# Performance work log

Measured on AMD Instinct MI355X. Metric: run time of the kernel, lower is better.

The kernel has to match this reference:

```python
import jax, jax.numpy as jnp
import numpy as np

T = 2048      # num_tokens = batch*seq
H = 2048      # hidden_size
E = 64        # num_experts
K = 8         # num_experts_per_tok (top_k)
I = 768       # moe_intermediate_size


def setup_inputs() -> dict:
    key = jax.random.key(0)
    k0, k1, k2, k3, k4 = jax.random.split(key, 5)
    scale = 0.02
    return {
        "hidden_states": jax.random.normal(k0, (T, H), jnp.float32),
        "w_router": jax.random.normal(k1, (E, H), jnp.float32) * scale,   # gate Linear [E, H]
        "w_gate": jax.random.normal(k2, (E, I, H), jnp.float32) * scale,  # per-expert gate_proj
        "w_up": jax.random.normal(k3, (E, I, H), jnp.float32) * scale,    # per-expert up_proj
        "w_down": jax.random.normal(k4, (E, H, I), jnp.float32) * scale,  # per-expert down_proj
    }


def reference(hidden_states, w_router, w_gate, w_up, w_down):
    x = hidden_states                                  # [T, H]
    num_tokens = x.shape[0]
    # --- router ---
    router_logits = x @ w_router.T                     # [T, E]
    probs = jax.nn.softmax(router_logits.astype(jnp.float32), axis=-1)
    top_w, top_i = jax.lax.top_k(probs, K)             # [T, K]
    top_w = top_w / jnp.sum(top_w, axis=-1, keepdims=True)  # norm_topk_prob
    top_w = top_w.astype(x.dtype)
    # dense combine weights [T, E], K nonzeros per row
    combine = jnp.zeros((num_tokens, E), x.dtype).at[
        jnp.arange(num_tokens)[:, None], top_i
    ].set(top_w)
    # --- experts: SwiGLU MLP per expert, weighted combine ---
    def body(acc, params):
        wg, wu, wd, w_e = params                       # [I,H], [I,H], [H,I], [T]
        h = jax.nn.silu(x @ wg.T) * (x @ wu.T)         # [T, I]
        return acc + w_e[:, None] * (h @ wd.T), None
    out, _ = jax.lax.scan(body, jnp.zeros_like(x), (w_gate, w_up, w_down, combine.T))
    return out
```

## Files before the change

kernel.cpp:

```cpp
#include <hip/hip_runtime.h>
#include <hip/hip_fp16.h>

#define T_TOK 2048
#define H_DIM 2048
#define E_NUM 64
#define TOPK  8
#define I_DIM 768

#define BK   32

#define GU_MT 3
#define GU_NT (I_DIM / 64)
#define GU_NWG (GU_MT * GU_NT * E_NUM)
#define DN_MT 3
#define DN_NT (H_DIM / 128)
#define DN_NWG (DN_MT * DN_NT * E_NUM)

using f16x8 = __attribute__((ext_vector_type(8))) _Float16;
using f16x4 = __attribute__((ext_vector_type(4))) _Float16;
using f16x2 = __attribute__((ext_vector_type(2))) _Float16;
using f32x4 = __attribute__((ext_vector_type(4))) float;

__device__ __forceinline__ f16x4 cvt4(float4 v) {
    f16x2 lo = __builtin_bit_cast(f16x2, __builtin_amdgcn_cvt_pkrtz(v.x, v.y));
    f16x2 hi = __builtin_bit_cast(f16x2, __builtin_amdgcn_cvt_pkrtz(v.z, v.w));
    f16x4 o;
    o[0] = lo[0]; o[1] = lo[1]; o[2] = hi[0]; o[3] = hi[1];
    return o;
}
__device__ __forceinline__ f16x8 cvt8(float4 a, float4 b) {
    f16x4 lo = cvt4(a), hi = cvt4(b);
    f16x8 r;
    r[0] = lo[0]; r[1] = lo[1]; r[2] = lo[2]; r[3] = lo[3];
    r[4] = hi[0]; r[5] = hi[1]; r[6] = hi[2]; r[7] = hi[3];
    return r;
}

__device__ __forceinline__ void gload16(const void* g, void* l) {
    __builtin_amdgcn_global_load_lds(
        (const __attribute__((address_space(1))) unsigned int*)g,
        (__attribute__((address_space(3))) unsigned int*)l,
        16, 0, 0);
}

__global__ void convert_x_kernel(const float* __restrict__ x, _Float16* __restrict__ xh, int n) {
    int i = (blockIdx.x * blockDim.x + threadIdx.x) * 4;
    if (i < n) {
        float4 v = *reinterpret_cast<const float4*>(x + i);
        *reinterpret_cast<f16x4*>(xh + i) = cvt4(v);
    }
}

__global__ __launch_bounds__(64) void router_topk_kernel(
        const float* __restrict__ x, const float* __restrict__ wr,
        int* __restrict__ topk_i, float* __restrict__ topk_w) {
    __shared__ float xs[H_DIM];
    int t = blockIdx.x;
    int lane = threadIdx.x;
    const float* xp = x + (size_t)t * H_DIM;
    for (int i = lane * 4; i < H_DIM; i += 64 * 4) {
        *reinterpret_cast<float4*>(xs + i) = *reinterpret_cast<const float4*>(xp + i);
    }
    __syncthreads();
    const float* wp = wr + (size_t)lane * H_DIM;
    float acc = 0.f;
    for (int h = 0; h < H_DIM; h += 4) {
        float4 w = *reinterpret_cast<const float4*>(wp + h);
        acc += xs[h] * w.x + xs[h + 1] * w.y + xs[h + 2] * w.z + xs[h + 3] * w.w;
    }
    float m = acc;
    #pragma unroll
    for (int d = 32; d; d >>= 1) m = fmaxf(m, __shfl_xor(m, d));
    float p = __expf(acc - m);
    float s = p;
    #pragma unroll
    for (int d = 32; d; d >>= 1) s += __shfl_xor(s, d);
    p /= s;
    float selv[TOPK]; int seli[TOPK];
    float cur = p;
    #pragma unroll
    for (int k = 0; k < TOPK; ++k) {
        float v = cur; int idx = lane;
        #pragma unroll
        for (int d = 32; d; d >>= 1) {
            float ov = __shfl_xor(v, d); int oi = __shfl_xor(idx, d);
            if (ov > v || (ov == v && oi < idx)) { v = ov; idx = oi; }
        }
        selv[k] = v; seli[k] = idx;
        if (lane == idx) cur = -1.f;
    }
    float sum = 0.f;
    #pragma unroll
    for (int k = 0; k < TOPK; ++k) sum += selv[k];
    if (lane == 0) {
        #pragma unroll
        for (int k = 0; k < TOPK; ++k) {
            topk_i[t * TOPK + k] = seli[k];
            topk_w[t * TOPK + k] = selv[k] / sum;
        }
    }
}

__global__ void count_kernel(const int* __restrict__ topk_i, int* __restrict__ counts) {
    int i = blockIdx.x * blockDim.x + threadIdx.x;
    if (i < T_TOK * TOPK) atomicAdd(&counts[topk_i[i]], 1);
}

__global__ __launch_bounds__(64) void scan_kernel(const int* __restrict__ counts,
                                                  int* __restrict__ offsets,
                                                  int* __restrict__ cursor) {
    __shared__ int c[E_NUM];
    int e = threadIdx.x;
    c[e] = counts[e];
    __syncthreads();
    int off = 0;
    for (int j = 0; j < e; ++j) off += c[j];
    offsets[e] = off;
    cursor[e] = off;
}

__global__ void scatter_kernel(const int* __restrict__ topk_i, const float* __restrict__ topk_w,
                               int* __restrict__ cursor,
                               int* __restrict__ token_list, float* __restrict__ weight_list) {
    int i = blockIdx.x * blockDim.x + threadIdx.x;
    if (i < T_TOK * TOPK) {
        int e = topk_i[i];
        int pos = atomicAdd(&cursor[e], 1);
        token_list[pos] = i >> 3;
        weight_list[pos] = topk_w[i];
    }
}

__global__ __launch_bounds__(256) void gateup_kernel(
        const _Float16* __restrict__ xh, const float* __restrict__ wg,
        const float* __restrict__ wu, const int* __restrict__ offsets,
        const int* __restrict__ counts, const int* __restrict__ token_list,
        _Float16* __restrict__ hbuf) {
    int orig = blockIdx.x;
    int w = (orig & 7) * (GU_NWG / 8) + (orig >> 3);
    int mt = w % GU_MT;
    int nt = (w / GU_MT) % GU_NT;
    int e  = w / (GU_MT * GU_NT);
    int n_e = counts[e];
    int off_e = offsets[e];
    int n_base = nt * 64;
    const float* wg_e = wg + (size_t)e * I_DIM * H_DIM;
    const float* wu_e = wu + (size_t)e * I_DIM * H_DIM;

    __shared__ __align__(16) _Float16 As[128 * 32];
    __shared__ __align__(16) float    Bgs[64 * 32];
    __shared__ __align__(16) float    Bus[64 * 32];
    __shared__ int toks[128];

    int tid = threadIdx.x;
    int ar = tid >> 2, aslot = tid & 3;
    int acf = aslot ^ (ar & 3);
    int brr = tid >> 3, bslot = tid & 7;
    int bcf = bslot ^ (brr & 7);
    const float* bg0 = wg_e + (size_t)(n_base + brr) * H_DIM + bcf * 4;
    const float* bg1 = wg_e + (size_t)(n_base + 32 + brr) * H_DIM + bcf * 4;
    const float* bu0 = wu_e + (size_t)(n_base + brr) * H_DIM + bcf * 4;
    const float* bu1 = wu_e + (size_t)(n_base + 32 + brr) * H_DIM + bcf * 4;

    int wave = tid >> 6, lane = tid & 63;
    int wm = wave >> 1, wn = wave & 1;
    int aoff[4];
    #pragma unroll
    for (int fm = 0; fm < 4; ++fm) {
        int row = wm * 64 + fm * 16 + (lane & 15);
        aoff[fm] = row * 32 + ((lane >> 4) ^ (lane & 3)) * 8;
    }
    int boff0[2], boff1[2];
    #pragma unroll
    for (int fn = 0; fn < 2; ++fn) {
        int row = wn * 32 + fn * 16 + (lane & 15);
        int c0 = (lane >> 4) * 2;
        boff0[fn] = row * 32 + (c0 ^ (lane & 7)) * 4;
        boff1[fn] = row * 32 + ((c0 + 1) ^ (lane & 7)) * 4;
    }

    for (int m_base = mt * 128; m_base < n_e; m_base += GU_MT * 128) {
        if (tid < 128) toks[tid] = token_list[off_e + min(m_base + tid, n_e - 1)];
        __syncthreads();
        const _Float16* asrc0 = xh + (size_t)toks[ar] * H_DIM + acf * 8;
        const _Float16* asrc1 = xh + (size_t)toks[64 + ar] * H_DIM + acf * 8;

        f32x4 accg[4][2], accu[4][2];
        #pragma unroll
        for (int i = 0; i < 4; ++i)
            #pragma unroll
            for (int j = 0; j < 2; ++j) { accg[i][j] = (f32x4)0.f; accu[i][j] = (f32x4)0.f; }

        for (int t = 0; t < H_DIM / BK; ++t) {
            int k0 = t * BK;
            gload16(asrc0 + k0, As + tid * 8);
            gload16(asrc1 + k0, As + 2048 + tid * 8);
            gload16(bg0 + k0, Bgs + tid * 4);
            gload16(bg1 + k0, Bgs + 1024 + tid * 4);
            gload16(bu0 + k0, Bus + tid * 4);
            gload16(bu1 + k0, Bus + 1024 + tid * 4);
            __syncthreads();
            f16x8 a[4];
            #pragma unroll
            for (int fm = 0; fm < 4; ++fm) a[fm] = *reinterpret_cast<const f16x8*>(&As[aoff[fm]]);
            #pragma unroll
            for (int fn = 0; fn < 2; ++fn) {
                float4 g0 = *reinterpret_cast<const float4*>(&Bgs[boff0[fn]]);
                float4 g1 = *reinterpret_cast<const float4*>(&Bgs[boff1[fn]]);
                float4 u0 = *reinterpret_cast<const float4*>(&Bus[boff0[fn]]);
                float4 u1 = *reinterpret_cast<const float4*>(&Bus[boff1[fn]]);
                f16x8 bgf = cvt8(g0, g1);
                f16x8 buf = cvt8(u0, u1);
                #pragma unroll
                for (int fm = 0; fm < 4; ++fm) {
                    accg[fm][fn] = __builtin_amdgcn_mfma_f32_16x16x32_f16(a[fm], bgf, accg[fm][fn], 0, 0, 0);
                    accu[fm][fn] = __builtin_amdgcn_mfma_f32_16x16x32_f16(a[fm], buf, accu[fm][fn], 0, 0, 0);
                }
            }
            __syncthreads();
        }

        #pragma unroll
        for (int fm = 0; fm < 4; ++fm) {
            #pragma unroll
            for (int reg = 0; reg < 4; ++reg) {
                int row = wm * 64 + fm * 16 + (lane >> 4) * 4 + reg;
                int m = m_base + row;
                if (m < n_e) {
                    #pragma unroll
                    for (int fn = 0; fn < 2; ++fn) {
                        int col = wn * 32 + fn * 16 + (lane & 15);
                        float g = accg[fm][fn][reg];
                        float u = accu[fm][fn][reg];
                        float hv = g * u / (1.f + __expf(-g));
                        hbuf[(size_t)(off_e + m) * I_DIM + n_base + col] = (_Float16)hv;
                    }
                }
            }
        }
        __syncthreads();
    }
}

__global__ __launch_bounds__(256) void down_kernel(
        const _Float16* __restrict__ hbuf, const float* __restrict__ wd,
        const int* __restrict__ offsets, const int* __restrict__ counts,
        const int* __restrict__ token_list, const float* __restrict__ weight_list,
        float* __restrict__ out) {
    int orig = blockIdx.x;
    int w = (orig & 7) * (DN_NWG / 8) + (orig >> 3);
    int mt = w % DN_MT;
    int nt = (w / DN_MT) % DN_NT;
    int e  = w / (DN_MT * DN_NT);
    int n_e = counts[e];
    int off_e = offsets[e];
    int n_base = nt * 128;
    const float* wd_e = wd + (size_t)e * H_DIM * I_DIM;

    __shared__ __align__(16) _Float16 As[128 * 32];
    __shared__ __align__(16) float    Bs[128 * 32];

    int tid = threadIdx.x;
    int ar = tid >> 2, aslot = tid & 3;
    int acf = aslot ^ (ar & 3);
    int brr = tid >> 3, bslot = tid & 7;
    int bcf = bslot ^ (brr & 7);
    const float* bs0 = wd_e + (size_t)(n_base + brr) * I_DIM + bcf * 4;
    const float* bs1 = bs0 + (size_t)32 * I_DIM;
    const float* bs2 = bs0 + (size_t)64 * I_DIM;
    const float* bs3 = bs0 + (size_t)96 * I_DIM;

    int wave = tid >> 6, lane = tid & 63;
    int wm = wave >> 1, wn = wave & 1;
    int aoff[4];
    #pragma unroll
    for (int fm = 0; fm < 4; ++fm) {
        int row = wm * 64 + fm * 16 + (lane & 15);
        aoff[fm] = row * 32 + ((lane >> 4) ^ (lane & 3)) * 8;
    }
    int boff0[4], boff1[4];
    #pragma unroll
    for (int fn = 0; fn < 4; ++fn) {
        int row = wn * 64 + fn * 16 + (lane & 15);
        int c0 = (lane >> 4) * 2;
        boff0[fn] = row * 32 + (c0 ^ (lane & 7)) * 4;
        boff1[fn] = row * 32 + ((c0 + 1) ^ (lane & 7)) * 4;
    }

    for (int m_base = mt * 128; m_base < n_e; m_base += DN_MT * 128) {
        int am0 = min(m_base + ar, n_e - 1);
        int am1 = min(m_base + 64 + ar, n_e - 1);
        const _Float16* asrc0 = hbuf + (size_t)(off_e + am0) * I_DIM + acf * 8;
        const _Float16* asrc1 = hbuf + (size_t)(off_e + am1) * I_DIM + acf * 8;

        f32x4 acc[4][4];
        #pragma unroll
        for (int i = 0; i < 4; ++i)
            #pragma unroll
            for (int j = 0; j < 4; ++j) acc[i][j] = (f32x4)0.f;

        for (int t = 0; t < I_DIM / BK; ++t) {
            int k0 = t * BK;
            gload16(asrc0 + k0, As + tid * 8);
            gload16(asrc1 + k0, As + 2048 + tid * 8);
            gload16(bs0 + k0, Bs + tid * 4);
            gload16(bs1 + k0, Bs + 1024 + tid * 4);
            gload16(bs2 + k0, Bs + 2048 + tid * 4);
            gload16(bs3 + k0, Bs + 3072 + tid * 4);
            __syncthreads();
            f16x8 a[4];
            #pragma unroll
            for (int fm = 0; fm < 4; ++fm) a[fm] = *reinterpret_cast<const f16x8*>(&As[aoff[fm]]);
            #pragma unroll
            for (int fn = 0; fn < 4; ++fn) {
                float4 v0 = *reinterpret_cast<const float4*>(&Bs[boff0[fn]]);
                float4 v1 = *reinterpret_cast<const float4*>(&Bs[boff1[fn]]);
                f16x8 bb = cvt8(v0, v1);
                #pragma unroll
                for (int fm = 0; fm < 4; ++fm)
                    acc[fm][fn] = __builtin_amdgcn_mfma_f32_16x16x32_f16(a[fm], bb, acc[fm][fn], 0, 0, 0);
            }
            __syncthreads();
        }

        #pragma unroll
        for (int fm = 0; fm < 4; ++fm) {
            #pragma unroll
            for (int reg = 0; reg < 4; ++reg) {
                int m = m_base + wm * 64 + fm * 16 + (lane >> 4) * 4 + reg;
                if (m < n_e) {
                    int slot = off_e + m;
                    int t = token_list[slot];
                    float wt = weight_list[slot];
                    float* orow = out + (size_t)t * H_DIM + n_base;
                    #pragma unroll
                    for (int fn = 0; fn < 4; ++fn) {
                        int col = wn * 64 + fn * 16 + (lane & 15);
                        atomicAdd(orow + col, wt * acc[fm][fn][reg]);
                    }
                }
            }
        }
        __syncthreads();
    }
}

extern "C" void kernel_launch(void* const* d_in, const int* in_sizes, int n_in,
                              void* d_out, int out_size, void* d_ws, size_t ws_size,
                              hipStream_t stream) {
    const float* x  = (const float*)d_in[0];
    const float* wr = (const float*)d_in[1];
    const float* wg = (const float*)d_in[2];
    const float* wu = (const float*)d_in[3];
    const float* wd = (const float*)d_in[4];
    float* out = (float*)d_out;

    char* p = (char*)d_ws;
    auto carve = [&](size_t bytes) { char* q = p; p += (bytes + 255) & ~255ULL; return q; };
    _Float16* xh     = (_Float16*)carve((size_t)T_TOK * H_DIM * 2);
    _Float16* hbuf   = (_Float16*)carve((size_t)T_TOK * TOPK * I_DIM * 2);
    int*   topk_i    = (int*)  carve(T_TOK * TOPK * 4);
    float* topk_w    = (float*)carve(T_TOK * TOPK * 4);
    int*   tlist     = (int*)  carve(T_TOK * TOPK * 4);
    float* wlist     = (float*)carve(T_TOK * TOPK * 4);
    int*   counts    = (int*)  carve(E_NUM * 4);
    int*   offsets   = (int*)  carve(E_NUM * 4);
    int*   cursor    = (int*)  carve(E_NUM * 4);

    (void)hipMemsetAsync(d_out, 0, (size_t)out_size * 4, stream);
    (void)hipMemsetAsync(counts, 0, E_NUM * 4, stream);

    convert_x_kernel<<<(T_TOK * H_DIM) / (256 * 4), 256, 0, stream>>>(x, xh, T_TOK * H_DIM);
    router_topk_kernel<<<T_TOK, 64, 0, stream>>>(x, wr, topk_i, topk_w);
    count_kernel<<<(T_TOK * TOPK) / 256, 256, 0, stream>>>(topk_i, counts);
    scan_kernel<<<1, 64, 0, stream>>>(counts, offsets, cursor);
    scatter_kernel<<<(T_TOK * TOPK) / 256, 256, 0, stream>>>(topk_i, topk_w, cursor, tlist, wlist);
    gateup_kernel<<<GU_NWG, 256, 0, stream>>>(xh, wg, wu, offsets, counts, tlist, hbuf);
    down_kernel<<<DN_NWG, 256, 0, stream>>>(hbuf, wd, offsets, counts, tlist, wlist, out);
}
```

Baseline: 704.5 us.

## Load GEMM operands directly from global into registers, drop LDS staging

The gate/up and down expert GEMM kernels no longer stage A and B tiles in shared memory through global_load_lds with barriers. Each wave now owns a column slice and loads its MFMA fragments straight from global memory into registers, covering 128 rows in eight 16-row fragments. This removes the per-K-step __syncthreads and LDS round trips. Blocks with no rows to process now exit early, and the M-tile count drops from 3 to 2. In exchange, A rows (gathered tokens) are read separately by every wave with no sharing through LDS, so global and L2 traffic rises and each load is a narrow strided access.

```diff
diff --git a/kernel.cpp b/kernel.cpp
--- a/kernel.cpp
+++ b/kernel.cpp
@@ -9,10 +9,10 @@
 
 #define BK   32
 
-#define GU_MT 3
+#define GU_MT 2
 #define GU_NT (I_DIM / 64)
 #define GU_NWG (GU_MT * GU_NT * E_NUM)
-#define DN_MT 3
+#define DN_MT 2
 #define DN_NT (H_DIM / 128)
 #define DN_NWG (DN_MT * DN_NT * E_NUM)
 
@@ -34,13 +34,6 @@
     r[0] = lo[0]; r[1] = lo[1]; r[2] = lo[2]; r[3] = lo[3];
     r[4] = hi[0]; r[5] = hi[1]; r[6] = hi[2]; r[7] = hi[3];
     return r;
-}
-
-__device__ __forceinline__ void gload16(const void* g, void* l) {
-    __builtin_amdgcn_global_load_lds(
-        (const __attribute__((address_space(1))) unsigned int*)g,
-        (__attribute__((address_space(3))) unsigned int*)l,
-        16, 0, 0);
 }
 
 __global__ void convert_x_kernel(const float* __restrict__ x, _Float16* __restrict__ xh, int n) {
@@ -142,103 +135,83 @@
     int nt = (w / GU_MT) % GU_NT;
     int e  = w / (GU_MT * GU_NT);
     int n_e = counts[e];
+    if (mt * 128 >= n_e) return;
     int off_e = offsets[e];
-    int n_base = nt * 64;
-    const float* wg_e = wg + (size_t)e * I_DIM * H_DIM;
-    const float* wu_e = wu + (size_t)e * I_DIM * H_DIM;
-
-    __shared__ __align__(16) _Float16 As[128 * 32];
-    __shared__ __align__(16) float    Bgs[64 * 32];
-    __shared__ __align__(16) float    Bus[64 * 32];
-    __shared__ int toks[128];
 
     int tid = threadIdx.x;
-    int ar = tid >> 2, aslot = tid & 3;
-    int acf = aslot ^ (ar & 3);
-    int brr = tid >> 3, bslot = tid & 7;
-    int bcf = bslot ^ (brr & 7);
-    const float* bg0 = wg_e + (size_t)(n_base + brr) * H_DIM + bcf * 4;
-    const float* bg1 = wg_e + (size_t)(n_base + 32 + brr) * H_DIM + bcf * 4;
-    const float* bu0 = wu_e + (size_t)(n_base + brr) * H_DIM + bcf * 4;
-    const float* bu1 = wu_e + (size_t)(n_base + 32 + brr) * H_DIM + bcf * 4;
-
-    int wave = tid >> 6, lane = tid & 63;
-    int wm = wave >> 1, wn = wave & 1;
-    int aoff[4];
-    #pragma unroll
-    for (int fm = 0; fm < 4; ++fm) {
-        int row = wm * 64 + fm * 16 + (lane & 15);
-        aoff[fm] = row * 32 + ((lane >> 4) ^ (lane & 3)) * 8;
-    }
-    int boff0[2], boff1[2];
-    #pragma unroll
-    for (int fn = 0; fn < 2; ++fn) {
-        int row = wn * 32 + fn * 16 + (lane & 15);
-        int c0 = (lane >> 4) * 2;
-        boff0[fn] = row * 32 + (c0 ^ (lane & 7)) * 4;
-        boff1[fn] = row * 32 + ((c0 + 1) ^ (lane & 7)) * 4;
-    }
+    int wn = tid >> 6, lane = tid & 63;
+    int lrow = lane & 15;
+    int kgrp = lane >> 4;
+    int colbase = nt * 64 + wn * 16;
+
+    const float* gp = wg + (size_t)e * I_DIM * H_DIM + (size_t)(colbase + lrow) * H_DIM + kgrp * 8;
+    const float* up = wu + (size_t)e * I_DIM * H_DIM + (size_t)(colbase + lrow) * H_DIM + kgrp * 8;
 
     for (int m_base = mt * 128; m_base < n_e; m_base += GU_MT * 128) {
-        if (tid < 128) toks[tid] = token_list[off_e + min(m_base + tid, n_e - 1)];
-        __syncthreads();
-        const _Float16* asrc0 = xh + (size_t)toks[ar] * H_DIM + acf * 8;
-        const _Float16* asrc1 = xh + (size_t)toks[64 + ar] * H_DIM + acf * 8;
-
-        f32x4 accg[4][2], accu[4][2];
-        #pragma unroll
-        for (int i = 0; i < 4; ++i)
+        const _Float16* ap0; const _Float16* ap1; const _Float16* ap2; const _Float16* ap3;
+        const _Float16* ap4; const _Float16* ap5; const _Float16* ap6; const _Float16* ap7;
+        {
+            const _Float16* tmp[8];
             #pragma unroll
-            for (int j = 0; j < 2; ++j) { accg[i][j] = (f32x4)0.f; accu[i][j] = (f32x4)0.f; }
-
-        for (int t = 0; t < H_DIM / BK; ++t) {
-            int k0 = t * BK;
-            gload16(asrc0 + k0, As + tid * 8);
-            gload16(asrc1 + k0, As + 2048 + tid * 8);
-            gload16(bg0 + k0, Bgs + tid * 4);
-            gload16(bg1 + k0, Bgs + 1024 + tid * 4);
-            gload16(bu0 + k0, Bus + tid * 4);
-            gload16(bu1 + k0, Bus + 1024 + tid * 4);
-            __syncthreads();
-            f16x8 a[4];
+            for (int fm = 0; fm < 8; ++fm) {
+                int m = min(m_base + fm * 16 + lrow, n_e - 1);
+                int tok = token_list[off_e + m];
+                tmp[fm] = xh + (size_t)tok * H_DIM + kgrp * 8;
+            }
+            ap0 = tmp[0]; ap1 = tmp[1]; ap2 = tmp[2]; ap3 = tmp[3];
+            ap4 = tmp[4]; ap5 = tmp[5]; ap6 = tmp[6]; ap7 = tmp[7];
+        }
+
+        f32x4 accg[8], accu[8];
+        #pragma unroll
+        for (int i = 0; i < 8; ++i) { accg[i] = (f32x4)0.f; accu[i] = (f32x4)0.f; }
+
+        for (int k0 = 0; k0 < H_DIM; k0 += BK) {
+            f16x8 a0 = *reinterpret_cast<const f16x8*>(ap0 + k0);
+            f16x8 a1 = *reinterpret_cast<const f16x8*>(ap1 + k0);
+            f16x8 a2 = *reinterpret_cast<const f16x8*>(ap2 + k0);
+            f16x8 a3 = *reinterpret_cast<const f16x8*>(ap3 + k0);
+            f16x8 a4 = *reinterpret_cast<const f16x8*>(ap4 + k0);
+            f16x8 a5 = *reinterpret_cast<const f16x8*>(ap5 + k0);
+            f16x8 a6 = *reinterpret_cast<const f16x8*>(ap6 + k0);
+            f16x8 a7 = *reinterpret_cast<const f16x8*>(ap7 + k0);
+            float4 g0 = *reinterpret_cast<const float4*>(gp + k0);
+            float4 g1 = *reinterpret_cast<const float4*>(gp + k0 + 4);
+            float4 u0 = *reinterpret_cast<const float4*>(up + k0);
+            float4 u1 = *reinterpret_cast<const float4*>(up + k0 + 4);
+            f16x8 bg = cvt8(g0, g1);
+            f16x8 bu = cvt8(u0, u1);
+            accg[0] = __builtin_amdgcn_mfma_f32_16x16x32_f16(a0, bg, accg[0], 0, 0, 0);
+            accu[0] = __builtin_amdgcn_mfma_f32_16x16x32_f16(a0, bu, accu[0], 0, 0, 0);
+            accg[1] = __builtin_amdgcn_mfma_f32_16x16x32_f16(a1, bg, accg[1], 0, 0, 0);
+            accu[1] = __builtin_amdgcn_mfma_f32_16x16x32_f16(a1, bu, accu[1], 0, 0, 0);
+            accg[2] = __builtin_amdgcn_mfma_f32_16x16x32_f16(a2, bg, accg[2], 0, 0, 0);
+            accu[2] = __builtin_amdgcn_mfma_f32_16x16x32_f16(a2, bu, accu[2], 0, 0, 0);
+            accg[3] = __builtin_amdgcn_mfma_f32_16x16x32_f16(a3, bg, accg[3], 0, 0, 0);
+            accu[3] = __builtin_amdgcn_mfma_f32_16x16x32_f16(a3, bu, accu[3], 0, 0, 0);
+            accg[4] = __builtin_amdgcn_mfma_f32_16x16x32_f16(a4, bg, accg[4], 0, 0, 0);
+            accu[4] = __builtin_amdgcn_mfma_f32_16x16x32_f16(a4, bu, accu[4], 0, 0, 0);
+            accg[5] = __builtin_amdgcn_mfma_f32_16x16x32_f16(a5, bg, accg[5], 0, 0, 0);
+            accu[5] = __builtin_amdgcn_mfma_f32_16x16x32_f16(a5, bu, accu[5], 0, 0, 0);
+            accg[6] = __builtin_amdgcn_mfma_f32_16x16x32_f16(a6, bg, accg[6], 0, 0, 0);
+            accu[6] = __builtin_amdgcn_mfma_f32_16x16x32_f16(a6, bu, accu[6], 0, 0, 0);
+            accg[7] = __builtin_amdgcn_mfma_f32_16x16x32_f16(a7, bg, accg[7], 0, 0, 0);
+            accu[7] = __builtin_amdgcn_mfma_f32_16x16x32_f16(a7, bu, accu[7], 0, 0, 0);
+        }
+
+        #pragma unroll
+        for (int fm = 0; fm < 8; ++fm) {
             #pragma unroll
-            for (int fm = 0; fm < 4; ++fm) a[fm] = *reinterpret_cast<const f16x8*>(&As[aoff[fm]]);
-            #pragma unroll
-            for (int fn = 0; fn < 2; ++fn) {
-                float4 g0 = *reinterpret_cast<const float4*>(&Bgs[boff0[fn]]);
-                float4 g1 = *reinterpret_cast<const float4*>(&Bgs[boff1[fn]]);
-                float4 u0 = *reinterpret_cast<const float4*>(&Bus[boff0[fn]]);
-                float4 u1 = *reinterpret_cast<const float4*>(&Bus[boff1[fn]]);
-                f16x8 bgf = cvt8(g0, g1);
-                f16x8 buf = cvt8(u0, u1);
-                #pragma unroll
-                for (int fm = 0; fm < 4; ++fm) {
-                    accg[fm][fn] = __builtin_amdgcn_mfma_f32_16x16x32_f16(a[fm], bgf, accg[fm][fn], 0, 0, 0);
-                    accu[fm][fn] = __builtin_amdgcn_mfma_f32_16x16x32_f16(a[fm], buf, accu[fm][fn], 0, 0, 0);
+            for (int reg = 0; reg < 4; ++reg) {
+                int m = m_base + fm * 16 + kgrp * 4 + reg;
+                if (m < n_e) {
+                    float g = accg[fm][reg];
+                    float u = accu[fm][reg];
+                    float hv = g * u / (1.f + __expf(-g));
+                    hbuf[(size_t)(off_e + m) * I_DIM + colbase + lrow] = (_Float16)hv;
                 }
             }
-            __syncthreads();
-        }
-
-        #pragma unroll
-        for (int fm = 0; fm < 4; ++fm) {
-            #pragma unroll
-            for (int reg = 0; reg < 4; ++reg) {
-                int row = wm * 64 + fm * 16 + (lane >> 4) * 4 + reg;
-                int m = m_base + row;
-                if (m < n_e) {
-                    #pragma unroll
-                    for (int fn = 0; fn < 2; ++fn) {
-                        int col = wn * 32 + fn * 16 + (lane & 15);
-                        float g = accg[fm][fn][reg];
-                        float u = accu[fm][fn][reg];
-                        float hv = g * u / (1.f + __expf(-g));
-                        hbuf[(size_t)(off_e + m) * I_DIM + n_base + col] = (_Float16)hv;
-                    }
-                }
-            }
-        }
-        __syncthreads();
+        }
     }
 }
 
@@ -253,95 +226,84 @@
     int nt = (w / DN_MT) % DN_NT;
     int e  = w / (DN_MT * DN_NT);
     int n_e = counts[e];
+    if (mt * 128 >= n_e) return;
     int off_e = offsets[e];
-    int n_base = nt * 128;
-    const float* wd_e = wd + (size_t)e * H_DIM * I_DIM;
-
-    __shared__ __align__(16) _Float16 As[128 * 32];
-    __shared__ __align__(16) float    Bs[128 * 32];
 
     int tid = threadIdx.x;
-    int ar = tid >> 2, aslot = tid & 3;
-    int acf = aslot ^ (ar & 3);
-    int brr = tid >> 3, bslot = tid & 7;
-    int bcf = bslot ^ (brr & 7);
-    const float* bs0 = wd_e + (size_t)(n_base + brr) * I_DIM + bcf * 4;
-    const float* bs1 = bs0 + (size_t)32 * I_DIM;
-    const float* bs2 = bs0 + (size_t)64 * I_DIM;
-    const float* bs3 = bs0 + (size_t)96 * I_DIM;
-
-    int wave = tid >> 6, lane = tid & 63;
-    int wm = wave >> 1, wn = wave & 1;
-    int aoff[4];
-    #pragma unroll
-    for (int fm = 0; fm < 4; ++fm) {
-        int row = wm * 64 + fm * 16 + (lane & 15);
-        aoff[fm] = row * 32 + ((lane >> 4) ^ (lane & 3)) * 8;
-    }
-    int boff0[4], boff1[4];
-    #pragma unroll
-    for (int fn = 0; fn < 4; ++fn) {
-        int row = wn * 64 + fn * 16 + (lane & 15);
-        int c0 = (lane >> 4) * 2;
-        boff0[fn] = row * 32 + (c0 ^ (lane & 7)) * 4;
-        boff1[fn] = row * 32 + ((c0 + 1) ^ (lane & 7)) * 4;
-    }
+    int wn = tid >> 6, lane = tid & 63;
+    int lrow = lane & 15;
+    int kgrp = lane >> 4;
+    int colbase = nt * 128 + wn * 32;
+
+    const float* bp0 = wd + (size_t)e * H_DIM * I_DIM + (size_t)(colbase + lrow) * I_DIM + kgrp * 8;
+    const float* bp1 = bp0 + (size_t)16 * I_DIM;
 
     for (int m_base = mt * 128; m_base < n_e; m_base += DN_MT * 128) {
-        int am0 = min(m_base + ar, n_e - 1);
-        int am1 = min(m_base + 64 + ar, n_e - 1);
-        const _Float16* asrc0 = hbuf + (size_t)(off_e + am0) * I_DIM + acf * 8;
-        const _Float16* asrc1 = hbuf + (size_t)(off_e + am1) * I_DIM + acf * 8;
-
-        f32x4 acc[4][4];
-        #pragma unroll
-        for (int i = 0; i < 4; ++i)
+        const _Float16* ap0; const _Float16* ap1; const _Float16* ap2; const _Float16* ap3;
+        const _Float16* ap4; const _Float16* ap5; const _Float16* ap6; const _Float16* ap7;
+        {
+            const _Float16* tmp[8];
             #pragma unroll
-            for (int j = 0; j < 4; ++j) acc[i][j] = (f32x4)0.f;
-
-        for (int t = 0; t < I_DIM / BK; ++t) {
-            int k0 = t * BK;
-            gload16(asrc0 + k0, As + tid * 8);
-            gload16(asrc1 + k0, As + 2048 + tid * 8);
-            gload16(bs0 + k0, Bs + tid * 4);
-            gload16(bs1 + k0, Bs + 1024 + tid * 4);
-            gload16(bs2 + k0, Bs + 2048 + tid * 4);
-            gload16(bs3 + k0, Bs + 3072 + tid * 4);
-            __syncthreads();
-            f16x8 a[4];
-            #pragma unroll
-            for (int fm = 0; fm < 4; ++fm) a[fm] = *reinterpret_cast<const f16x8*>(&As[aoff[fm]]);
-            #pragma unroll
-            for (int fn = 0; fn < 4; ++fn) {
-                float4 v0 = *reinterpret_cast<const float4*>(&Bs[boff0[fn]]);
-                float4 v1 = *reinterpret_cast<const float4*>(&Bs[boff1[fn]]);
-                f16x8 bb = cvt8(v0, v1);
-                #pragma unroll
-                for (int fm = 0; fm < 4; ++fm)
-                    acc[fm][fn] = __builtin_amdgcn_mfma_f32_16x16x32_f16(a[fm], bb, acc[fm][fn], 0, 0, 0);
+            for (int fm = 0; fm < 8; ++fm) {
+                int m = min(m_base + fm * 16 + lrow, n_e - 1);
+                tmp[fm] = hbuf + (size_t)(off_e + m) * I_DIM + kgrp * 8;
             }
-            __syncthreads();
-        }
-
-        #pragma unroll
-        for (int fm = 0; fm < 4; ++fm) {
+            ap0 = tmp[0]; ap1 = tmp[1]; ap2 = tmp[2]; ap3 = tmp[3];
+            ap4 = tmp[4]; ap5 = tmp[5]; ap6 = tmp[6]; ap7 = tmp[7];
+        }
+
+        f32x4 acc0[8], acc1[8];
+        #pragma unroll
+        for (int i = 0; i < 8; ++i) { acc0[i] = (f32x4)0.f; acc1[i] = (f32x4)0.f; }
+
+        for (int k0 = 0; k0 < I_DIM; k0 += BK) {
+            f16x8 a0 = *reinterpret_cast<const f16x8*>(ap0 + k0);
+            f16x8 a1 = *reinterpret_cast<const f16x8*>(ap1 + k0);
+            f16x8 a2 = *reinterpret_cast<const f16x8*>(ap2 + k0);
+            f16x8 a3 = *reinterpret_cast<const f16x8*>(ap3 + k0);
+            f16x8 a4 = *reinterpret_cast<const f16x8*>(ap4 + k0);
+            f16x8 a5 = *reinterpret_cast<const f16x8*>(ap5 + k0);
+            f16x8 a6 = *reinterpret_cast<const f16x8*>(ap6 + k0);
+            f16x8 a7 = *reinterpret_cast<const f16x8*>(ap7 + k0);
+            float4 v00 = *reinterpret_cast<const float4*>(bp0 + k0);
+            float4 v01 = *reinterpret_cast<const float4*>(bp0 + k0 + 4);
+            float4 v10 = *reinterpret_cast<const float4*>(bp1 + k0);
+            float4 v11 = *reinterpret_cast<const float4*>(bp1 + k0 + 4);
+            f16x8 b0 = cvt8(v00, v01);
+            f16x8 b1 = cvt8(v10, v11);
+            acc0[0] = __builtin_amdgcn_mfma_f32_16x16x32_f16(a0, b0, acc0[0], 0, 0, 0);
+            acc1[0] = __builtin_amdgcn_mfma_f32_16x16x32_f16(a0, b1, acc1[0], 0, 0, 0);
+            acc0[1] = __builtin_amdgcn_mfma_f32_16x16x32_f16(a1, b0, acc0[1], 0, 0, 0);
+            acc1[1] = __builtin_amdgcn_mfma_f32_16x16x32_f16(a1, b1, acc1[1], 0, 0, 0);
+            acc0[2] = __builtin_amdgcn_mfma_f32_16x16x32_f16(a2, b0, acc0[2], 0, 0, 0);
+            acc1[2] = __builtin_amdgcn_mfma_f32_16x16x32_f16(a2, b1, acc1[2], 0, 0, 0);
+            acc0[3] = __builtin_amdgcn_mfma_f32_16x16x32_f16(a3, b0, acc0[3], 0, 0, 0);
+            acc1[3] = __builtin_amdgcn_mfma_f32_16x16x32_f16(a3, b1, acc1[3], 0, 0, 0);
+            acc0[4] = __builtin_amdgcn_mfma_f32_16x16x32_f16(a4, b0, acc0[4], 0, 0, 0);
+            acc1[4] = __builtin_amdgcn_mfma_f32_16x16x32_f16(a4, b1, acc1[4], 0, 0, 0);
+            acc0[5] = __builtin_amdgcn_mfma_f32_16x16x32_f16(a5, b0, acc0[5], 0, 0, 0);
+            acc1[5] = __builtin_amdgcn_mfma_f32_16x16x32_f16(a5, b1, acc1[5], 0, 0, 0);
+            acc0[6] = __builtin_amdgcn_mfma_f32_16x16x32_f16(a6, b0, acc0[6], 0, 0, 0);
+            acc1[6] = __builtin_amdgcn_mfma_f32_16x16x32_f16(a6, b1, acc1[6], 0, 0, 0);
+            acc0[7] = __builtin_amdgcn_mfma_f32_16x16x32_f16(a7, b0, acc0[7], 0, 0, 0);
+            acc1[7] = __builtin_amdgcn_mfma_f32_16x16x32_f16(a7, b1, acc1[7], 0, 0, 0);
+        }
+
+        #pragma unroll
+        for (int fm = 0; fm < 8; ++fm) {
             #pragma unroll
             for (int reg = 0; reg < 4; ++reg) {
-                int m = m_base + wm * 64 + fm * 16 + (lane >> 4) * 4 + reg;
+                int m = m_base + fm * 16 + kgrp * 4 + reg;
                 if (m < n_e) {
                     int slot = off_e + m;
                     int t = token_list[slot];
                     float wt = weight_list[slot];
-                    float* orow = out + (size_t)t * H_DIM + n_base;
-                    #pragma unroll
-                    for (int fn = 0; fn < 4; ++fn) {
-                        int col = wn * 64 + fn * 16 + (lane & 15);
-                        atomicAdd(orow + col, wt * acc[fm][fn][reg]);
-                    }
+                    float* orow = out + (size_t)t * H_DIM;
+                    atomicAdd(orow + colbase + lrow,      wt * acc0[fm][reg]);
+                    atomicAdd(orow + colbase + 16 + lrow, wt * acc1[fm][reg]);
                 }
             }
         }
-        __syncthreads();
     }
 }
 
```

New measurement: 1.389 ms. 1.97x slower.

## Replace atomic combine in down projection with slot buffer and per-token reduce

Applied to the files above, without the earlier changes.

The down-projection kernel now writes weighted per-slot outputs as fp16 into a [T*K, H] buffer instead of doing float atomicAdds into the output. A new reduce kernel gathers each token's K slots through an inverse-slot map built in scatter and writes the output directly, which also removes the output memset. This trades atomic contention and read-modify-write traffic for an extra 64MB fp16 write plus read and one more launch, and it adds fp16 rounding before the reduction.

```diff
diff --git a/kernel.cpp b/kernel.cpp
--- a/kernel.cpp
+++ b/kernel.cpp
@@ -121,13 +121,15 @@
 
 __global__ void scatter_kernel(const int* __restrict__ topk_i, const float* __restrict__ topk_w,
                                int* __restrict__ cursor,
-                               int* __restrict__ token_list, float* __restrict__ weight_list) {
+                               int* __restrict__ token_list, float* __restrict__ weight_list,
+                               int* __restrict__ inv_slot) {
     int i = blockIdx.x * blockDim.x + threadIdx.x;
     if (i < T_TOK * TOPK) {
         int e = topk_i[i];
         int pos = atomicAdd(&cursor[e], 1);
         token_list[pos] = i >> 3;
         weight_list[pos] = topk_w[i];
+        inv_slot[i] = pos;
     }
 }
 
@@ -246,7 +248,7 @@
         const _Float16* __restrict__ hbuf, const float* __restrict__ wd,
         const int* __restrict__ offsets, const int* __restrict__ counts,
         const int* __restrict__ token_list, const float* __restrict__ weight_list,
-        float* __restrict__ out) {
+        _Float16* __restrict__ ybuf) {
     int orig = blockIdx.x;
     int w = (orig & 7) * (DN_NWG / 8) + (orig >> 3);
     int mt = w % DN_MT;
@@ -330,19 +332,43 @@
                 int m = m_base + wm * 64 + fm * 16 + (lane >> 4) * 4 + reg;
                 if (m < n_e) {
                     int slot = off_e + m;
-                    int t = token_list[slot];
                     float wt = weight_list[slot];
-                    float* orow = out + (size_t)t * H_DIM + n_base;
+                    _Float16* yrow = ybuf + (size_t)slot * H_DIM + n_base;
                     #pragma unroll
                     for (int fn = 0; fn < 4; ++fn) {
                         int col = wn * 64 + fn * 16 + (lane & 15);
-                        atomicAdd(orow + col, wt * acc[fm][fn][reg]);
+                        yrow[col] = (_Float16)(wt * acc[fm][fn][reg]);
                     }
                 }
             }
         }
         __syncthreads();
     }
+}
+
+__global__ __launch_bounds__(256) void reduce_kernel(
+        const _Float16* __restrict__ ybuf, const int* __restrict__ inv_slot,
+        float* __restrict__ out) {
+    int t = blockIdx.x;
+    int c = threadIdx.x * 8;
+    int s[TOPK];
+    #pragma unroll
+    for (int k = 0; k < TOPK; ++k) s[k] = inv_slot[t * TOPK + k];
+    float sum[8];
+    #pragma unroll
+    for (int j = 0; j < 8; ++j) sum[j] = 0.f;
+    #pragma unroll
+    for (int k = 0; k < TOPK; ++k) {
+        f16x8 v = *reinterpret_cast<const f16x8*>(ybuf + (size_t)s[k] * H_DIM + c);
+        #pragma unroll
+        for (int j = 0; j < 8; ++j) sum[j] += (float)v[j];
+    }
+    float* orow = out + (size_t)t * H_DIM + c;
+    float4 o0, o1;
+    o0.x = sum[0]; o0.y = sum[1]; o0.z = sum[2]; o0.w = sum[3];
+    o1.x = sum[4]; o1.y = sum[5]; o1.z = sum[6]; o1.w = sum[7];
+    *reinterpret_cast<float4*>(orow) = o0;
+    *reinterpret_cast<float4*>(orow + 4) = o1;
 }
 
 extern "C" void kernel_launch(void* const* d_in, const int* in_sizes, int n_in,
@@ -359,22 +385,24 @@
     auto carve = [&](size_t bytes) { char* q = p; p += (bytes + 255) & ~255ULL; return q; };
     _Float16* xh     = (_Float16*)carve((size_t)T_TOK * H_DIM * 2);
     _Float16* hbuf   = (_Float16*)carve((size_t)T_TOK * TOPK * I_DIM * 2);
+    _Float16* ybuf   = (_Float16*)carve((size_t)T_TOK * TOPK * H_DIM * 2);
     int*   topk_i    = (int*)  carve(T_TOK * TOPK * 4);
     float* topk_w    = (float*)carve(T_TOK * TOPK * 4);
     int*   tlist     = (int*)  carve(T_TOK * TOPK * 4);
     float* wlist     = (float*)carve(T_TOK * TOPK * 4);
+    int*   inv_slot  = (int*)  carve(T_TOK * TOPK * 4);
     int*   counts    = (int*)  carve(E_NUM * 4);
     int*   offsets   = (int*)  carve(E_NUM * 4);
     int*   cursor    = (int*)  carve(E_NUM * 4);
 
-    (void)hipMemsetAsync(d_out, 0, (size_t)out_size * 4, stream);
     (void)hipMemsetAsync(counts, 0, E_NUM * 4, stream);
 
     convert_x_kernel<<<(T_TOK * H_DIM) / (256 * 4), 256, 0, stream>>>(x, xh, T_TOK * H_DIM);
     router_topk_kernel<<<T_TOK, 64, 0, stream>>>(x, wr, topk_i, topk_w);
     count_kernel<<<(T_TOK * TOPK) / 256, 256, 0, stream>>>(topk_i, counts);
     scan_kernel<<<1, 64, 0, stream>>>(counts, offsets, cursor);
-    scatter_kernel<<<(T_TOK * TOPK) / 256, 256, 0, stream>>>(topk_i, topk_w, cursor, tlist, wlist);
+    scatter_kernel<<<(T_TOK * TOPK) / 256, 256, 0, stream>>>(topk_i, topk_w, cursor, tlist, wlist, inv_slot);
     gateup_kernel<<<GU_NWG, 256, 0, stream>>>(xh, wg, wu, offsets, counts, tlist, hbuf);
-    down_kernel<<<DN_NWG, 256, 0, stream>>>(hbuf, wd, offsets, counts, tlist, wlist, out);
-}
+    down_kernel<<<DN_NWG, 256, 0, stream>>>(hbuf, wd, offsets, counts, tlist, wlist, ybuf);
+    reduce_kernel<<<T_TOK, 256, 0, stream>>>(ybuf, inv_slot, out);
+}
```

Measured after the change: 659.4 us, median of 3. 6.4% less time.
